# Optimization experiments

Hardware: AMD Instinct MI355X
Metric: run time of the kernel (lower is better)

Reference implementation:

```python
import jax, jax.numpy as jnp
import numpy as np

N_NODES = 50000   # nodes in the graph (rows of x)
N_ENT = 100000    # entity embedding vocab
E = 800000        # edges (avg degree 16)
D = 100           # hidden dim (hard-coded in the torch module)
R = 100           # num_relations*2
B = 10            # num_bases


def setup_inputs() -> dict:
    key = jax.random.key(0)
    ks = jax.random.split(key, 9)
    inp = {}
    inp["entity"] = jax.random.randint(ks[0], (N_NODES,), 0, N_ENT, dtype=jnp.int32)
    inp["edge_index"] = jax.random.randint(ks[1], (2, E), 0, N_NODES, dtype=jnp.int32)
    inp["edge_type"] = jax.random.randint(ks[2], (E,), 0, R, dtype=jnp.int32)
    inp["edge_norm"] = jax.random.uniform(ks[3], (E,), dtype=jnp.float32)
    inp["emb"] = jax.random.normal(ks[4], (N_ENT, D), dtype=jnp.float32) * 0.02
    s = 1.0 / np.sqrt(B * D)  # uniform(num_bases*in_channels) init bound
    for i, l in enumerate(("1", "2", "3")):
        k = jax.random.split(ks[5 + i], 4)
        inp["basis" + l] = jax.random.uniform(k[0], (B, D, D), minval=-s, maxval=s, dtype=jnp.float32)
        inp["att" + l] = jax.random.uniform(k[1], (R, B), minval=-s, maxval=s, dtype=jnp.float32)
        inp["root" + l] = jax.random.uniform(k[2], (D, D), minval=-s, maxval=s, dtype=jnp.float32)
        inp["bias" + l] = jax.random.uniform(k[3], (D,), minval=-s, maxval=s, dtype=jnp.float32)
    return inp


def rgcn_conv(x, src, dst, edge_type, edge_norm, basis, att, root, bias):
    # message: m_e = (x[src_e] @ W[edge_type_e]) * edge_norm_e, with
    # W[r] = sum_b att[r, b] * basis[b].
    # Compute per-node basis projections once, then combine per-edge with
    # relation coefficients (avoids materializing [E, D, D] weights).
    n = x.shape[0]
    num_bases = basis.shape[0]
    H = jnp.einsum('ni,bio->nbo', x, basis)              # [N, B, D]
    coef = att[edge_type] * edge_norm[:, None]           # [E, B]
    msg = jnp.zeros((src.shape[0], basis.shape[2]), x.dtype)
    for b in range(num_bases):                           # small fixed loop
        msg = msg + coef[:, b:b + 1] * jnp.take(H[:, b, :], src, axis=0)
    # scatter-mean over target nodes (PyG aggr='mean')
    ones = jnp.ones((src.shape[0],), x.dtype)
    deg = jax.ops.segment_sum(ones, dst, num_segments=n)
    aggr = jax.ops.segment_sum(msg, dst, num_segments=n) / jnp.maximum(deg, 1.0)[:, None]
    return aggr + x @ root + bias


def reference(entity, edge_index, edge_type, edge_norm, emb,
              basis1, att1, root1, bias1,
              basis2, att2, root2, bias2,
              basis3, att3, root3, bias3):
    src, dst = edge_index[0], edge_index[1]
    x = jnp.take(emb, entity, axis=0)  # entity embedding lookup [N, D]
    # dropout is identity at inference).
    x1 = rgcn_conv(x, src, dst, edge_type, edge_norm, basis1, att1, root1, bias1)
    x = jax.nn.relu(rgcn_conv(x1, src, dst, edge_type, edge_norm, basis1, att1, root1, bias1))
    x2 = rgcn_conv(x, src, dst, edge_type, edge_norm, basis2, att2, root2, bias2)
    x = jax.nn.relu(rgcn_conv(x2, src, dst, edge_type, edge_norm, basis1, att1, root1, bias1))
    x3 = rgcn_conv(x, src, dst, edge_type, edge_norm, basis3, att3, root3, bias3)
    return x3
```

## Files before the change

kernel.cpp:

```cpp
#include <hip/hip_runtime.h>


#define DIMD 100
#define NBASES 10
#define KTOT 1100
#define KC 32
#define NCHUNK 35
#define KPAD 1120
#define BTPLANE (128 * KPAD)
#define BTSIZE (3 * BTPLANE)

typedef __attribute__((ext_vector_type(8))) short short8;
typedef __attribute__((ext_vector_type(4))) float floatx4;

static inline size_t align256(size_t x) { return (x + 255) & ~(size_t)255; }

__device__ inline unsigned short f2bf_rne(float f) {
    unsigned u = __float_as_uint(f);
    unsigned r = u + 0x7FFFu + ((u >> 16) & 1u);
    return (unsigned short)(r >> 16);
}
__device__ inline float bf2f(unsigned short h) {
    return __uint_as_float(((unsigned)h) << 16);
}


__global__ __launch_bounds__(256) void hist_kernel(const int* __restrict__ dst,
                                                   int* __restrict__ counts, int E) {
    int e = blockIdx.x * 256 + threadIdx.x;
    if (e < E) atomicAdd(&counts[dst[e]], 1);
}

__global__ __launch_bounds__(1024) void scan_kernel(const int* __restrict__ counts,
                                                    int* __restrict__ row_ptr,
                                                    int* __restrict__ next_pos, int n) {
    __shared__ int part[1024];
    __shared__ int base_s[1024];
    int t = threadIdx.x;
    int chunk = (n + 1023) / 1024;
    int lo = t * chunk, hi = min(lo + chunk, n);
    int s = 0;
    for (int i = lo; i < hi; ++i) s += counts[i];
    part[t] = s;
    __syncthreads();
    if (t == 0) {
        int run = 0;
        for (int i = 0; i < 1024; ++i) { int v = part[i]; base_s[i] = run; run += v; }
        row_ptr[n] = run;
    }
    __syncthreads();
    int run = base_s[t];
    for (int i = lo; i < hi; ++i) {
        row_ptr[i] = run;
        next_pos[i] = run;
        run += counts[i];
    }
}

__global__ __launch_bounds__(256) void scatter_kernel(
        const int* __restrict__ src, const int* __restrict__ dst,
        const int* __restrict__ etype, const float* __restrict__ enorm,
        const int* __restrict__ counts, int* __restrict__ next_pos,
        int* __restrict__ ssrc, int* __restrict__ stype, float* __restrict__ snid, int E) {
    int e = blockIdx.x * 256 + threadIdx.x;
    if (e < E) {
        int d = dst[e];
        int pos = atomicAdd(&next_pos[d], 1);
        ssrc[pos] = src[e];
        stype[pos] = etype[e];
        float deg = (float)max(counts[d], 1);
        snid[pos] = enorm[e] / deg;
    }
}

__global__ __launch_bounds__(256) void gather_kernel(const int* __restrict__ entity,
                                                     const float* __restrict__ emb,
                                                     float* __restrict__ x, int total) {
    int i = blockIdx.x * 256 + threadIdx.x;
    if (i < total) {
        int n = i / DIMD;
        int d = i - n * DIMD;
        x[i] = emb[(size_t)entity[n] * DIMD + d];
    }
}

__global__ __launch_bounds__(256) void transposeB_kernel(
        const float* __restrict__ Bm,
        const float* __restrict__ root,
        unsigned short* __restrict__ Bt) {
    int col = blockIdx.x;
    for (int k = threadIdx.x; k < KPAD; k += 256) {
        float v = 0.f;
        if (col < DIMD && k < KTOT)
            v = (k < 1000) ? Bm[(size_t)k * DIMD + col]
                           : root[(size_t)(k - 1000) * DIMD + col];
        unsigned short h = f2bf_rne(v);  float r  = v - bf2f(h);
        unsigned short m = f2bf_rne(r);  float r2 = r - bf2f(m);
        unsigned short l = f2bf_rne(r2);
        size_t o = (size_t)col * KPAD + k;
        Bt[o] = h;
        Bt[BTPLANE + o] = m;
        Bt[2 * BTPLANE + o] = l;
    }
}


__global__ __launch_bounds__(256) void phaseA_kernel(
        const float* __restrict__ x, const int* __restrict__ row_ptr,
        const int* __restrict__ ssrc, const int* __restrict__ stype,
        const float* __restrict__ snid, const float* __restrict__ att,
        float* __restrict__ S, int N) {
    __shared__ float att_s[1000];
    for (int i = threadIdx.x; i < 1000; i += 256) att_s[i] = att[i];
    __syncthreads();

    int wave = threadIdx.x >> 6;
    int l = threadIdx.x & 63;
    int n = blockIdx.x * 4 + wave;
    if (n >= N) return;

    int e0 = row_ptr[n], e1 = row_ptr[n + 1];
    float acc0[NBASES];
    float acc1[NBASES];
#pragma unroll
    for (int b = 0; b < NBASES; ++b) { acc0[b] = 0.f; acc1[b] = 0.f; }
    bool hi = (l < DIMD - 64);

    int t_cur = 0; float nv_cur = 0.f, xa = 0.f, xb = 0.f;
    if (e0 < e1) {
        int s0 = ssrc[e0];
        t_cur = stype[e0];
        nv_cur = snid[e0];
        const float* xr = x + (size_t)s0 * DIMD;
        xa = xr[l];
        xb = hi ? xr[64 + l] : 0.f;
    }
    for (int e = e0; e < e1; ++e) {
        int t_nxt = 0; float nv_nxt = 0.f, xa_n = 0.f, xb_n = 0.f;
        if (e + 1 < e1) {
            int sn = ssrc[e + 1];
            t_nxt = stype[e + 1];
            nv_nxt = snid[e + 1];
            const float* xr = x + (size_t)sn * DIMD;
            xa_n = xr[l];
            xb_n = hi ? xr[64 + l] : 0.f;
        }
        const float* ar = att_s + t_cur * NBASES;
#pragma unroll
        for (int b = 0; b < NBASES; ++b) {
            float c = ar[b] * nv_cur;
            acc0[b] += c * xa;
            acc1[b] += c * xb;
        }
        t_cur = t_nxt; nv_cur = nv_nxt; xa = xa_n; xb = xb_n;
    }
    float* Sr = S + (size_t)n * (NBASES * DIMD);
#pragma unroll
    for (int b = 0; b < NBASES; ++b) {
        Sr[b * DIMD + l] = acc0[b];
        if (hi) Sr[b * DIMD + 64 + l] = acc1[b];
    }
}


__global__ __launch_bounds__(256, 3) void phaseB_kernel(
        const float* __restrict__ S, const float* __restrict__ x,
        const unsigned short* __restrict__ Bt,
        const float* __restrict__ bias, float* __restrict__ out,
        int N, int do_relu) {
    __shared__ short Ah[64][40], Am[64][40], Al[64][40];
    __shared__ short Bh[128][40], Bmm[128][40], Bl[128][40];

    int tid = threadIdx.x;
    int w = tid >> 6, l = tid & 63;
    int lr = l & 15, kg8 = (l >> 4) * 8;
    int n0 = blockIdx.x * 64;

    int arow = tid >> 2, akq = tid & 3;
    int gr = min(n0 + arow, N - 1);
    const float* Sr = S + (size_t)gr * 1000;
    const float* xr = x + (size_t)gr * DIMD;

    floatx4 acc[4][2];
#pragma unroll
    for (int rf = 0; rf < 4; ++rf)
#pragma unroll
        for (int cf = 0; cf < 2; ++cf) acc[rf][cf] = (floatx4)(0.f);

    for (int c = 0; c < NCHUNK; ++c) {
        int k0 = c * KC;
        __syncthreads();

        {
            int kgb = k0 + akq * 8;
            float4 va = make_float4(0.f, 0.f, 0.f, 0.f), vb = va;
            if (kgb < 1000)      va = *(const float4*)(Sr + kgb);
            else if (kgb < KTOT) va = *(const float4*)(xr + (kgb - 1000));
            int kgb2 = kgb + 4;
            if (kgb2 < 1000)      vb = *(const float4*)(Sr + kgb2);
            else if (kgb2 < KTOT) vb = *(const float4*)(xr + (kgb2 - 1000));
            float v[8] = {va.x, va.y, va.z, va.w, vb.x, vb.y, vb.z, vb.w};
            short8 ph, pm, pl;
#pragma unroll
            for (int i = 0; i < 8; ++i) {
                unsigned short h = f2bf_rne(v[i]);  float r  = v[i] - bf2f(h);
                unsigned short m = f2bf_rne(r);     float r2 = r - bf2f(m);
                unsigned short lo = f2bf_rne(r2);
                ph[i] = (short)h; pm[i] = (short)m; pl[i] = (short)lo;
            }
            *(short8*)&Ah[arow][akq * 8] = ph;
            *(short8*)&Am[arow][akq * 8] = pm;
            *(short8*)&Al[arow][akq * 8] = pl;
        }
#pragma unroll
        for (int lv = 0; lv < 3; ++lv) {
            const unsigned short* plane = Bt + (size_t)lv * BTPLANE;
#pragma unroll
            for (int i = 0; i < 2; ++i) {
                int idx = tid + i * 256;
                int col = idx >> 2, kq = idx & 3;
                short8 vB = *(const short8*)(plane + (size_t)col * KPAD + k0 + kq * 8);
                short* dstL = (lv == 0) ? &Bh[col][kq * 8]
                             : (lv == 1) ? &Bmm[col][kq * 8] : &Bl[col][kq * 8];
                *(short8*)dstL = vB;
            }
        }
        __syncthreads();

        short8 bh[2], bm[2], bl[2];
#pragma unroll
        for (int cf = 0; cf < 2; ++cf) {
            int bc = w * 32 + cf * 16 + lr;
            bh[cf] = *(const short8*)&Bh[bc][kg8];
            bm[cf] = *(const short8*)&Bmm[bc][kg8];
            bl[cf] = *(const short8*)&Bl[bc][kg8];
        }
#pragma unroll
        for (int rf = 0; rf < 4; ++rf) {
            int ar = rf * 16 + lr;
            short8 ah = *(const short8*)&Ah[ar][kg8];
            short8 am = *(const short8*)&Am[ar][kg8];
            short8 al = *(const short8*)&Al[ar][kg8];
#pragma unroll
            for (int cf = 0; cf < 2; ++cf) {
                floatx4 a = acc[rf][cf];
                a = __builtin_amdgcn_mfma_f32_16x16x32_bf16(ah, bh[cf], a, 0, 0, 0);
                a = __builtin_amdgcn_mfma_f32_16x16x32_bf16(ah, bm[cf], a, 0, 0, 0);
                a = __builtin_amdgcn_mfma_f32_16x16x32_bf16(am, bh[cf], a, 0, 0, 0);
                a = __builtin_amdgcn_mfma_f32_16x16x32_bf16(ah, bl[cf], a, 0, 0, 0);
                a = __builtin_amdgcn_mfma_f32_16x16x32_bf16(al, bh[cf], a, 0, 0, 0);
                a = __builtin_amdgcn_mfma_f32_16x16x32_bf16(am, bm[cf], a, 0, 0, 0);
                acc[rf][cf] = a;
            }
        }
    }

#pragma unroll
    for (int rf = 0; rf < 4; ++rf) {
#pragma unroll
        for (int cf = 0; cf < 2; ++cf) {
            int cidx = w * 32 + cf * 16 + lr;
            if (cidx < DIMD) {
                float bs = bias[cidx];
#pragma unroll
                for (int j = 0; j < 4; ++j) {
                    int r = n0 + rf * 16 + (l >> 4) * 4 + j;
                    if (r < N) {
                        float v = acc[rf][cf][j] + bs;
                        if (do_relu) v = fmaxf(v, 0.f);
                        out[(size_t)r * DIMD + cidx] = v;
                    }
                }
            }
        }
    }
}


extern "C" void kernel_launch(void* const* d_in, const int* in_sizes, int n_in,
                              void* d_out, int out_size, void* d_ws, size_t ws_size,
                              hipStream_t stream) {
    const int* entity = (const int*)d_in[0];
    const int* edge_index = (const int*)d_in[1];
    const int* edge_type = (const int*)d_in[2];
    const float* edge_norm = (const float*)d_in[3];
    const float* emb = (const float*)d_in[4];
    const float* basisP[3] = {(const float*)d_in[5], (const float*)d_in[9], (const float*)d_in[13]};
    const float* attP[3]   = {(const float*)d_in[6], (const float*)d_in[10], (const float*)d_in[14]};
    const float* rootP[3]  = {(const float*)d_in[7], (const float*)d_in[11], (const float*)d_in[15]};
    const float* biasP[3]  = {(const float*)d_in[8], (const float*)d_in[12], (const float*)d_in[16]};

    const int N = in_sizes[0];
    const int E = in_sizes[1] / 2;
    const int* src = edge_index;
    const int* dst = edge_index + E;

    char* w = (char*)d_ws;
    float* S = (float*)w;            w += align256((size_t)N * NBASES * DIMD * 4);
    float* X0 = (float*)w;           w += align256((size_t)N * DIMD * 4);
    float* X1 = (float*)w;           w += align256((size_t)N * DIMD * 4);
    int* counts = (int*)w;           w += align256((size_t)N * 4);
    int* row_ptr = (int*)w;          w += align256((size_t)(N + 1) * 4);
    int* next_pos = (int*)w;         w += align256((size_t)N * 4);
    int* ssrc = (int*)w;             w += align256((size_t)E * 4);
    int* stype = (int*)w;            w += align256((size_t)E * 4);
    float* snid = (float*)w;         w += align256((size_t)E * 4);

    unsigned short* Bt0 = (unsigned short*)d_out;
    unsigned short* Bt1 = Bt0 + BTSIZE;
    unsigned short* Bt2 = (unsigned short*)X1;

    hipMemsetAsync(counts, 0, (size_t)N * 4, stream);
    int gE = (E + 255) / 256;
    hist_kernel<<<gE, 256, 0, stream>>>(dst, counts, E);
    scan_kernel<<<1, 1024, 0, stream>>>(counts, row_ptr, next_pos, N);
    scatter_kernel<<<gE, 256, 0, stream>>>(src, dst, edge_type, edge_norm, counts,
                                           next_pos, ssrc, stype, snid, E);
    int totalX = N * DIMD;
    gather_kernel<<<(totalX + 255) / 256, 256, 0, stream>>>(entity, emb, X0, totalX);

    transposeB_kernel<<<128, 256, 0, stream>>>(basisP[0], rootP[0], Bt0);
    transposeB_kernel<<<128, 256, 0, stream>>>(basisP[1], rootP[1], Bt1);

    const int relu[5] = {0, 1, 0, 1, 0};
    float* bufin[5]  = {X0, X1, X0, X1, X0};
    float* bufout[5] = {X1, X0, X1, X0, (float*)d_out};
    unsigned short* btP[5] = {Bt0, Bt0, Bt1, Bt0, Bt2};
    const float* attL[5]  = {attP[0], attP[0], attP[1], attP[0], attP[2]};
    const float* biasL[5] = {biasP[0], biasP[0], biasP[1], biasP[0], biasP[2]};

    int gA = (N + 3) / 4;
    int gB = (N + 63) / 64;
    for (int lyr = 0; lyr < 5; ++lyr) {
        if (lyr == 4)
            transposeB_kernel<<<128, 256, 0, stream>>>(basisP[2], rootP[2], Bt2);
        phaseA_kernel<<<gA, 256, 0, stream>>>(bufin[lyr], row_ptr, ssrc, stype, snid,
                                              attL[lyr], S, N);
        phaseB_kernel<<<gB, 256, 0, stream>>>(S, bufin[lyr], btP[lyr], biasL[lyr],
                                              bufout[lyr], N, relu[lyr]);
    }
}
```

Measured before the change: 1.573 ms.

## Batch edge gathers by four, truncate bf16 splits, hoist B loads before conversion

```diff
diff --git a/kernel.cpp b/kernel.cpp
--- a/kernel.cpp
+++ b/kernel.cpp
@@ -126,33 +126,30 @@
     for (int b = 0; b < NBASES; ++b) { acc0[b] = 0.f; acc1[b] = 0.f; }
     bool hi = (l < DIMD - 64);
 
-    int t_cur = 0; float nv_cur = 0.f, xa = 0.f, xb = 0.f;
-    if (e0 < e1) {
-        int s0 = ssrc[e0];
-        t_cur = stype[e0];
-        nv_cur = snid[e0];
-        const float* xr = x + (size_t)s0 * DIMD;
-        xa = xr[l];
-        xb = hi ? xr[64 + l] : 0.f;
-    }
-    for (int e = e0; e < e1; ++e) {
-        int t_nxt = 0; float nv_nxt = 0.f, xa_n = 0.f, xb_n = 0.f;
-        if (e + 1 < e1) {
-            int sn = ssrc[e + 1];
-            t_nxt = stype[e + 1];
-            nv_nxt = snid[e + 1];
-            const float* xr = x + (size_t)sn * DIMD;
-            xa_n = xr[l];
-            xb_n = hi ? xr[64 + l] : 0.f;
-        }
-        const float* ar = att_s + t_cur * NBASES;
-#pragma unroll
-        for (int b = 0; b < NBASES; ++b) {
-            float c = ar[b] * nv_cur;
-            acc0[b] += c * xa;
-            acc1[b] += c * xb;
-        }
-        t_cur = t_nxt; nv_cur = nv_nxt; xa = xa_n; xb = xb_n;
+    for (int e = e0; e < e1; e += 4) {
+        float xa[4], xb[4], nv[4];
+        int tt[4];
+#pragma unroll
+        for (int j = 0; j < 4; ++j) {
+            if (e + j < e1) {
+                int s = ssrc[e + j];
+                tt[j] = stype[e + j];
+                nv[j] = snid[e + j];
+                const float* xr = x + (size_t)s * DIMD;
+                xa[j] = xr[l];
+                xb[j] = hi ? xr[64 + l] : 0.f;
+            } else { tt[j] = 0; nv[j] = 0.f; xa[j] = 0.f; xb[j] = 0.f; }
+        }
+#pragma unroll
+        for (int j = 0; j < 4; ++j) {
+            const float* ar = att_s + tt[j] * NBASES;
+#pragma unroll
+            for (int b = 0; b < NBASES; ++b) {
+                float c = ar[b] * nv[j];
+                acc0[b] += c * xa[j];
+                acc1[b] += c * xb[j];
+            }
+        }
     }
     float* Sr = S + (size_t)n * (NBASES * DIMD);
 #pragma unroll
@@ -191,27 +188,15 @@
         int k0 = c * KC;
         __syncthreads();
 
-        {
-            int kgb = k0 + akq * 8;
-            float4 va = make_float4(0.f, 0.f, 0.f, 0.f), vb = va;
-            if (kgb < 1000)      va = *(const float4*)(Sr + kgb);
-            else if (kgb < KTOT) va = *(const float4*)(xr + (kgb - 1000));
-            int kgb2 = kgb + 4;
-            if (kgb2 < 1000)      vb = *(const float4*)(Sr + kgb2);
-            else if (kgb2 < KTOT) vb = *(const float4*)(xr + (kgb2 - 1000));
-            float v[8] = {va.x, va.y, va.z, va.w, vb.x, vb.y, vb.z, vb.w};
-            short8 ph, pm, pl;
-#pragma unroll
-            for (int i = 0; i < 8; ++i) {
-                unsigned short h = f2bf_rne(v[i]);  float r  = v[i] - bf2f(h);
-                unsigned short m = f2bf_rne(r);     float r2 = r - bf2f(m);
-                unsigned short lo = f2bf_rne(r2);
-                ph[i] = (short)h; pm[i] = (short)m; pl[i] = (short)lo;
-            }
-            *(short8*)&Ah[arow][akq * 8] = ph;
-            *(short8*)&Am[arow][akq * 8] = pm;
-            *(short8*)&Al[arow][akq * 8] = pl;
-        }
+        int kgb = k0 + akq * 8;
+        float4 va = make_float4(0.f, 0.f, 0.f, 0.f), vb = va;
+        if (kgb < 1000)      va = *(const float4*)(Sr + kgb);
+        else if (kgb < KTOT) va = *(const float4*)(xr + (kgb - 1000));
+        int kgb2 = kgb + 4;
+        if (kgb2 < 1000)      vb = *(const float4*)(Sr + kgb2);
+        else if (kgb2 < KTOT) vb = *(const float4*)(xr + (kgb2 - 1000));
+
+        short8 vB[6];
 #pragma unroll
         for (int lv = 0; lv < 3; ++lv) {
             const unsigned short* plane = Bt + (size_t)lv * BTPLANE;
@@ -219,10 +204,42 @@
             for (int i = 0; i < 2; ++i) {
                 int idx = tid + i * 256;
                 int col = idx >> 2, kq = idx & 3;
-                short8 vB = *(const short8*)(plane + (size_t)col * KPAD + k0 + kq * 8);
+                vB[lv * 2 + i] = *(const short8*)(plane + (size_t)col * KPAD + k0 + kq * 8);
+            }
+        }
+
+        {
+            float v[8] = {va.x, va.y, va.z, va.w, vb.x, vb.y, vb.z, vb.w};
+            unsigned hU[4], mU[4], lU[4];
+#pragma unroll
+            for (int i = 0; i < 4; ++i) {
+                float a = v[2 * i], b = v[2 * i + 1];
+                unsigned ua = __float_as_uint(a), ub = __float_as_uint(b);
+                float ha = __uint_as_float(ua & 0xFFFF0000u);
+                float hb = __uint_as_float(ub & 0xFFFF0000u);
+                hU[i] = (ua >> 16) | (ub & 0xFFFF0000u);
+                float ra = a - ha, rb = b - hb;
+                unsigned ura = __float_as_uint(ra), urb = __float_as_uint(rb);
+                float ma = __uint_as_float(ura & 0xFFFF0000u);
+                float mb = __uint_as_float(urb & 0xFFFF0000u);
+                mU[i] = (ura >> 16) | (urb & 0xFFFF0000u);
+                float r2a = ra - ma, r2b = rb - mb;
+                unsigned u2a = __float_as_uint(r2a), u2b = __float_as_uint(r2b);
+                lU[i] = (u2a >> 16) | (u2b & 0xFFFF0000u);
+            }
+            *(uint4*)&Ah[arow][akq * 8] = make_uint4(hU[0], hU[1], hU[2], hU[3]);
+            *(uint4*)&Am[arow][akq * 8] = make_uint4(mU[0], mU[1], mU[2], mU[3]);
+            *(uint4*)&Al[arow][akq * 8] = make_uint4(lU[0], lU[1], lU[2], lU[3]);
+        }
+#pragma unroll
+        for (int lv = 0; lv < 3; ++lv) {
+#pragma unroll
+            for (int i = 0; i < 2; ++i) {
+                int idx = tid + i * 256;
+                int col = idx >> 2, kq = idx & 3;
                 short* dstL = (lv == 0) ? &Bh[col][kq * 8]
                              : (lv == 1) ? &Bmm[col][kq * 8] : &Bl[col][kq * 8];
-                *(short8*)dstL = vB;
+                *(short8*)dstL = vB[lv * 2 + i];
             }
         }
         __syncthreads();
```

New measurement: 1.606 ms. 1.02x slower.
